# Kernel tuning notes

Hardware: AMD Instinct MI355X
Metric: run time of the kernel (lower is better)

## Reference

```python
import jax, jax.numpy as jnp
import numpy as np

WINDOW_SIZE = 11
SIGMA = 1.5
C1 = 0.01 ** 2
C2 = 0.03 ** 2


def _gaussian_window(window_size=WINDOW_SIZE, sigma=SIGMA):
    coords = jnp.arange(window_size, dtype=jnp.float32) - window_size // 2
    g = jnp.exp(-(coords ** 2) / (2.0 * sigma ** 2))
    g = g / g.sum()
    w3d = g[:, None, None] * g[None, :, None] * g[None, None, :]
    w3d = w3d / w3d.sum()
    return w3d[None, None]  # [1, 1, K, K, K] (OIDHW)


def _gconv3d(x, window):
    # depthwise 3D conv, SAME padding (pad = K//2), groups = C
    C = x.shape[1]
    w = jnp.broadcast_to(window, (C, 1) + window.shape[2:])
    pad = window.shape[-1] // 2
    return jax.lax.conv_general_dilated(
        x, w,
        window_strides=(1, 1, 1),
        padding=[(pad, pad)] * 3,
        dimension_numbers=("NCDHW", "OIDHW", "NCDHW"),
        feature_group_count=C,
    )


def setup_inputs() -> dict:
    key = jax.random.key(0)
    k1, k2 = jax.random.split(key)
    shape = (4, 1, 64, 192, 192)  # [B, C, D, H, W]
    pred = jax.random.uniform(k1, shape, dtype=jnp.float32)
    target = jax.random.uniform(k2, shape, dtype=jnp.float32)
    return {"pred": pred, "target": target}


def reference(pred, target):
    window = _gaussian_window()
    mu_p = _gconv3d(pred, window)
    mu_t = _gconv3d(target, window)
    mu_p_sq = mu_p ** 2
    mu_t_sq = mu_t ** 2
    mu_pt = mu_p * mu_t
    sigma_p_sq = _gconv3d(pred ** 2, window) - mu_p_sq
    sigma_t_sq = _gconv3d(target ** 2, window) - mu_t_sq
    sigma_pt = _gconv3d(pred * target, window) - mu_pt
    ssim_map = ((2.0 * mu_pt + C1) * (2.0 * sigma_pt + C2)) / (
        (mu_p_sq + mu_t_sq + C1) * (sigma_p_sq + sigma_t_sq + C2)
    )
    return 1.0 - ssim_map.mean()
```

## Files before the change

### kernel.cpp

```cpp
#include <hip/hip_runtime.h>


#define D_DIM 64
#define H_DIM 192
#define W_DIM 192
#define SLICE (H_DIM * W_DIM)
#define VOL   (D_DIM * SLICE)
#define NB    4
#define KS    11
#define RAD   5
#define TIL   16
#define HLO   26
#define SP    48
#define IPX   6
#define C1F   (0.01f * 0.01f)
#define C2F   (0.03f * 0.03f)

typedef _Float16 h2v __attribute__((ext_vector_type(2)));

__device__ __forceinline__ void make_window(float* g) {
    float s = 0.f;
#pragma unroll
    for (int i = 0; i < KS; ++i) {
        float c = (float)(i - RAD);
        g[i] = expf(-(c * c) * (1.0f / 4.5f));
        s += g[i];
    }
    float inv = 1.0f / s;
#pragma unroll
    for (int i = 0; i < KS; ++i) g[i] *= inv;
}

#define SSIM_ACC(MP, MT, E2, T2, PT) do {                                 \
    float _mps = (MP) * (MP), _mts = (MT) * (MT), _mpt = (MP) * (MT);     \
    float _num = (2.f * _mpt + C1F) * (2.f * ((PT) - _mpt) + C2F);        \
    float _den = (_mps + _mts + C1F) *                                    \
                 (((E2) - _mps) + ((T2) - _mts) + C2F);                   \
    ssim_sum += _num * __builtin_amdgcn_rcpf(_den);                       \
} while (0)

__global__ __launch_bounds__(256) void fused_ssim_kernel(
    const float* __restrict__ pred, const float* __restrict__ targ,
    float* __restrict__ partials) {
    __shared__ float spb[HLO * SP];
    __shared__ float stb[HLO * SP];
    __shared__ __attribute__((aligned(16))) _Float16 interm[HLO * TIL * IPX];
    __shared__ float red[4];

    float g[KS];
    make_window(g);

    const int tid = threadIdx.x;
    const int h0 = (blockIdx.x / 12) * TIL;
    const int w0 = (blockIdx.x % 12) * TIL;
    const int half = blockIdx.y;
    const float* pb = pred + (size_t)blockIdx.z * VOL;
    const float* tb = targ + (size_t)blockIdx.z * VOL;
    const int q0 = half ? 27 : 0;
    const int q1 = half ? 63 : 36;
    const int d_lo = half ? 32 : 0;
    const int d_hi = half ? 63 : 31;

    int sidx[3], slds[3];
    bool sa[3], sv[3];
#pragma unroll
    for (int k = 0; k < 3; ++k) {
        int i = tid + 256 * k;
        sa[k] = i < HLO * HLO;
        int y = i / HLO, x = i - y * HLO;
        int gh = h0 + y - RAD, gw = w0 + x - RAD;
        sv[k] = sa[k] && (unsigned)gh < (unsigned)H_DIM &&
                (unsigned)gw < (unsigned)W_DIM;
        sidx[k] = gh * W_DIM + gw;
        slds[k] = y * SP + x;
    }
    const int py = tid >> 4, px = tid & 15;

    float a0[KS], a1[KS], a2[KS], a3[KS], a4[KS];
#pragma unroll
    for (int j = 0; j < KS; ++j)
        a0[j] = a1[j] = a2[j] = a3[j] = a4[j] = 0.f;
    float ssim_sum = 0.f;

    float rp[3], rt[3];
    {
        const float* pq = pb + q0 * SLICE;
        const float* tq = tb + q0 * SLICE;
#pragma unroll
        for (int k = 0; k < 3; ++k) {
            rp[k] = sv[k] ? pq[sidx[k]] : 0.f;
            rt[k] = sv[k] ? tq[sidx[k]] : 0.f;
        }
    }

    for (int q = q0;; ++q) {
        __syncthreads();
#pragma unroll
        for (int k = 0; k < 3; ++k)
            if (sa[k]) { spb[slds[k]] = rp[k]; stb[slds[k]] = rt[k]; }
        if (q < q1) {
            const float* pn = pb + (q + 1) * SLICE;
            const float* tn = tb + (q + 1) * SLICE;
#pragma unroll
            for (int k = 0; k < 3; ++k) {
                rp[k] = sv[k] ? pn[sidx[k]] : 0.f;
                rt[k] = sv[k] ? tn[sidx[k]] : 0.f;
            }
        }
        __syncthreads();

#pragma unroll
        for (int it = 0; it < 2; ++it) {
            int t = tid + it * 256;
            if (t < HLO * TIL) {
                int r = t >> 4, c = t & 15;
                const float* pr = spb + r * SP + c;
                const float* tr = stb + r * SP + c;
                float s0 = 0.f, s1 = 0.f, s2 = 0.f, s3 = 0.f, s4 = 0.f;
#pragma unroll
                for (int k = 0; k < KS; ++k) {
                    float pv = pr[k], tv = tr[k], gk = g[k];
                    s0 += gk * pv;
                    s1 += gk * tv;
                    s2 += gk * pv * pv;
                    s3 += gk * tv * tv;
                    s4 += gk * pv * tv;
                }
                _Float16* ip = interm + t * IPX;
                h2v w01, w23;
                w01[0] = (_Float16)s0; w01[1] = (_Float16)s1;
                w23[0] = (_Float16)s2; w23[1] = (_Float16)s3;
                *(h2v*)ip = w01;
                *(h2v*)(ip + 2) = w23;
                ip[4] = (_Float16)s4;
            }
        }
        __syncthreads();

        {
            const _Float16* cb = interm + px * IPX;
            float v0 = 0.f, v1 = 0.f, v2 = 0.f, v3 = 0.f, v4 = 0.f;
#pragma unroll
            for (int k = 0; k < KS; ++k) {
                const _Float16* p = cb + (py + k) * (TIL * IPX);
                h2v w01 = *(const h2v*)p;
                h2v w23 = *(const h2v*)(p + 2);
                float gk = g[k];
                v0 += gk * (float)w01[0];
                v1 += gk * (float)w01[1];
                v2 += gk * (float)w23[0];
                v3 += gk * (float)w23[1];
                v4 += gk * (float)p[4];
            }
#pragma unroll
            for (int j = 0; j < KS; ++j) {
                float wj = g[10 - j];
                a0[j] += wj * v0; a1[j] += wj * v1; a2[j] += wj * v2;
                a3[j] += wj * v3; a4[j] += wj * v4;
            }
            if (q - 5 >= d_lo)
                SSIM_ACC(a0[0], a1[0], a2[0], a3[0], a4[0]);
#pragma unroll
            for (int j = 0; j < KS - 1; ++j) {
                a0[j] = a0[j + 1]; a1[j] = a1[j + 1]; a2[j] = a2[j + 1];
                a3[j] = a3[j + 1]; a4[j] = a4[j + 1];
            }
            a0[10] = 0.f; a1[10] = 0.f; a2[10] = 0.f; a3[10] = 0.f; a4[10] = 0.f;
        }
        if (q == q1) break;
    }

#pragma unroll
    for (int j = 0; j < 5; ++j) {
        int d = q1 - 4 + j;
        if (d >= d_lo && d <= d_hi)
            SSIM_ACC(a0[j], a1[j], a2[j], a3[j], a4[j]);
    }

    float a = ssim_sum;
#pragma unroll
    for (int off = 32; off > 0; off >>= 1) a += __shfl_down(a, off, 64);
    int lane = tid & 63, wv = tid >> 6;
    if (lane == 0) red[wv] = a;
    __syncthreads();
    if (tid == 0)
        partials[((blockIdx.z * 2 + blockIdx.y) * 144) + blockIdx.x] =
            red[0] + red[1] + red[2] + red[3];
}

__global__ __launch_bounds__(256) void finalize_kernel(
    const float* __restrict__ partials, int n, float* __restrict__ out) {
    double a = 0.0;
    for (int i = threadIdx.x; i < n; i += 256) a += (double)partials[i];
#pragma unroll
    for (int off = 32; off > 0; off >>= 1) a += __shfl_down(a, off, 64);
    __shared__ double red[4];
    int lane = threadIdx.x & 63, wv = threadIdx.x >> 6;
    if (lane == 0) red[wv] = a;
    __syncthreads();
    if (threadIdx.x == 0) {
        double s = red[0] + red[1] + red[2] + red[3];
        out[0] = (float)(1.0 - s / (double)((long long)NB * VOL));
    }
}

extern "C" void kernel_launch(void* const* d_in, const int* in_sizes, int n_in,
                              void* d_out, int out_size, void* d_ws, size_t ws_size,
                              hipStream_t stream) {
    const float* pred = (const float*)d_in[0];
    const float* targ = (const float*)d_in[1];
    float* out = (float*)d_out;
    float* partials = (float*)d_ws;

    fused_ssim_kernel<<<dim3(144, 2, NB), 256, 0, stream>>>(pred, targ, partials);
    finalize_kernel<<<1, 256, 0, stream>>>(partials, NB * 288, out);
}
```

Before: 225.8 us.

## Interleave pred/target in LDS, pack intermediates as padded 16-byte vectors, drop barrier

Pred and target halo tiles are stored as interleaved float2 in one shared array, so the horizontal pass needs one LDS load per tap instead of two. The five horizontal partial sums are packed into a 16-byte half-precision vector per pixel, with rows padded to 17 entries to spread banks, so the vertical pass does one wide LDS read per tap. The barrier at the top of the depth loop is removed; this relies on the two remaining barriers per iteration to order reuse of the shared buffers. The padded vectors waste three half-precision slots per pixel, which adds LDS footprint and write bandwidth.

```diff
diff --git a/kernel.cpp b/kernel.cpp
--- a/kernel.cpp
+++ b/kernel.cpp
@@ -11,12 +11,12 @@
 #define RAD   5
 #define TIL   16
 #define HLO   26
-#define SP    48
-#define IPX   6
+#define SP2   28
+#define IPP   17
 #define C1F   (0.01f * 0.01f)
 #define C2F   (0.03f * 0.03f)
 
-typedef _Float16 h2v __attribute__((ext_vector_type(2)));
+typedef _Float16 h8 __attribute__((ext_vector_type(8)));
 
 __device__ __forceinline__ void make_window(float* g) {
     float s = 0.f;
@@ -42,9 +42,8 @@
 __global__ __launch_bounds__(256) void fused_ssim_kernel(
     const float* __restrict__ pred, const float* __restrict__ targ,
     float* __restrict__ partials) {
-    __shared__ float spb[HLO * SP];
-    __shared__ float stb[HLO * SP];
-    __shared__ __attribute__((aligned(16))) _Float16 interm[HLO * TIL * IPX];
+    __shared__ float2 spt[HLO * SP2];
+    __shared__ h8 interm[HLO * IPP];
     __shared__ float red[4];
 
     float g[KS];
@@ -72,7 +71,7 @@
         sv[k] = sa[k] && (unsigned)gh < (unsigned)H_DIM &&
                 (unsigned)gw < (unsigned)W_DIM;
         sidx[k] = gh * W_DIM + gw;
-        slds[k] = y * SP + x;
+        slds[k] = y * SP2 + x;
     }
     const int py = tid >> 4, px = tid & 15;
 
@@ -94,10 +93,9 @@
     }
 
     for (int q = q0;; ++q) {
-        __syncthreads();
 #pragma unroll
         for (int k = 0; k < 3; ++k)
-            if (sa[k]) { spb[slds[k]] = rp[k]; stb[slds[k]] = rt[k]; }
+            if (sa[k]) spt[slds[k]] = make_float2(rp[k], rt[k]);
         if (q < q1) {
             const float* pn = pb + (q + 1) * SLICE;
             const float* tn = tb + (q + 1) * SLICE;
@@ -114,43 +112,40 @@
             int t = tid + it * 256;
             if (t < HLO * TIL) {
                 int r = t >> 4, c = t & 15;
-                const float* pr = spb + r * SP + c;
-                const float* tr = stb + r * SP + c;
+                const float2* pr = spt + r * SP2 + c;
                 float s0 = 0.f, s1 = 0.f, s2 = 0.f, s3 = 0.f, s4 = 0.f;
 #pragma unroll
                 for (int k = 0; k < KS; ++k) {
-                    float pv = pr[k], tv = tr[k], gk = g[k];
+                    float2 v = pr[k];
+                    float pv = v.x, tv = v.y, gk = g[k];
                     s0 += gk * pv;
                     s1 += gk * tv;
                     s2 += gk * pv * pv;
                     s3 += gk * tv * tv;
                     s4 += gk * pv * tv;
                 }
-                _Float16* ip = interm + t * IPX;
-                h2v w01, w23;
-                w01[0] = (_Float16)s0; w01[1] = (_Float16)s1;
-                w23[0] = (_Float16)s2; w23[1] = (_Float16)s3;
-                *(h2v*)ip = w01;
-                *(h2v*)(ip + 2) = w23;
-                ip[4] = (_Float16)s4;
+                h8 o;
+                o[0] = (_Float16)s0; o[1] = (_Float16)s1;
+                o[2] = (_Float16)s2; o[3] = (_Float16)s3;
+                o[4] = (_Float16)s4;
+                o[5] = (_Float16)0.f; o[6] = (_Float16)0.f; o[7] = (_Float16)0.f;
+                interm[r * IPP + c] = o;
             }
         }
         __syncthreads();
 
         {
-            const _Float16* cb = interm + px * IPX;
+            const h8* cp = interm + px;
             float v0 = 0.f, v1 = 0.f, v2 = 0.f, v3 = 0.f, v4 = 0.f;
 #pragma unroll
             for (int k = 0; k < KS; ++k) {
-                const _Float16* p = cb + (py + k) * (TIL * IPX);
-                h2v w01 = *(const h2v*)p;
-                h2v w23 = *(const h2v*)(p + 2);
+                h8 w = cp[(py + k) * IPP];
                 float gk = g[k];
-                v0 += gk * (float)w01[0];
-                v1 += gk * (float)w01[1];
-                v2 += gk * (float)w23[0];
-                v3 += gk * (float)w23[1];
-                v4 += gk * (float)p[4];
+                v0 += gk * (float)w[0];
+                v1 += gk * (float)w[1];
+                v2 += gk * (float)w[2];
+                v3 += gk * (float)w[3];
+                v4 += gk * (float)w[4];
             }
 #pragma unroll
             for (int j = 0; j < KS; ++j) {
```

Result: no change. 227.8 us (+0.9%).
